# Performance work log

Measured on AMD Instinct MI355X. Metric: run time of the kernel, lower is better.

Reference implementation:

```python
import jax, jax.numpy as jnp
import numpy as np

B, R, U, D = 16, 2048, 2048, 1024
EPS_ATT = 1e-8
EPS_LN = 1e-6


def setup_inputs() -> dict:
    key = jax.random.key(0)
    ks = jax.random.split(key, 6)
    s = 1.0 / np.sqrt(D)
    return {
        "Q": jax.random.normal(ks[0], (B, R, D), dtype=jnp.float32),
        "K": jax.random.normal(ks[1], (B, U, D), dtype=jnp.float32),
        "V": jax.random.normal(ks[2], (B, U, D), dtype=jnp.float32),
        "W1": jax.random.normal(ks[3], (D, D), dtype=jnp.float32) * s,
        "b1": jnp.zeros((D,), dtype=jnp.float32),
        "W2": jax.random.normal(ks[4], (D, D), dtype=jnp.float32) * s,
        "b2": jnp.zeros((D,), dtype=jnp.float32),
        "gamma": jnp.ones((D,), dtype=jnp.float32),
        "beta": jnp.zeros((D,), dtype=jnp.float32),
    }


def reference(Q, K, V, W1, b1, W2, b2, gamma, beta):
    d_model = Q.shape[-1]
    # Faithful to source: sqrt(d_model + epsilon)
    scale = jnp.sqrt(jnp.asarray(d_model, jnp.float32) + EPS_ATT)
    scores = jnp.einsum('brd,bud->bru', Q, K) / scale  # [B,R,U]
    att = jax.nn.softmax(scores, axis=-1)
    V_att = jnp.einsum('bru,bud->brd', att, V)  # [B,R,D]

    def layer_norm(x):
        mu = jnp.mean(x, axis=-1, keepdims=True)
        var = jnp.mean(jnp.square(x - mu), axis=-1, keepdims=True)
        return gamma * (x - mu) / jnp.sqrt(var + EPS_LN) + beta

    X = layer_norm(Q + V_att)
    ffn = jnp.maximum(X @ W1 + b1, 0.0) @ W2 + b2
    return layer_norm(ffn + X)
```

## Files before the change

### kernel.cpp

```cpp
#include <hip/hip_runtime.h>
#include <math.h>
#include <stdint.h>

#define BATCH 16
#define RDIM 2048
#define UDIM 2048
#define DDIM 1024

typedef __attribute__((ext_vector_type(8))) short short8;
typedef __attribute__((ext_vector_type(4))) float f32x4;
typedef __attribute__((ext_vector_type(8))) unsigned short ushort8;
typedef __attribute__((ext_vector_type(4))) unsigned short ushort4v;
typedef __attribute__((ext_vector_type(4))) float float4v;

__device__ __forceinline__ float bf2f(unsigned short u) {
  unsigned int x = ((unsigned int)u) << 16;
  return __builtin_bit_cast(float, x);
}
__device__ __forceinline__ unsigned short f2bf(float f) {
  unsigned int x = __builtin_bit_cast(unsigned int, f);
  unsigned int r = (x + 0x7fffu + ((x >> 16) & 1u)) >> 16;
  return (unsigned short)r;
}

__device__ __forceinline__ void gload_lds16(const void* g, void* l) {
  __builtin_amdgcn_global_load_lds(
      (const __attribute__((address_space(1))) void*)(uintptr_t)g,
      (__attribute__((address_space(3))) void*)(uint32_t)(uintptr_t)l,
      16, 0, 0);
}


__global__ __launch_bounds__(256) void k_conv_bf16(const float* __restrict__ in,
                                                   unsigned short* __restrict__ out,
                                                   float scale) {
  const long i = ((long)blockIdx.x * 256 + threadIdx.x) * 8;
  float4v a = *(const float4v*)(in + i);
  float4v b = *(const float4v*)(in + i + 4);
  ushort8 o;
#pragma unroll
  for (int j = 0; j < 4; ++j) o[j] = f2bf(a[j] * scale);
#pragma unroll
  for (int j = 0; j < 4; ++j) o[4 + j] = f2bf(b[j] * scale);
  *(ushort8*)(out + i) = o;
}

__global__ void k_transpose_bf16(const float* __restrict__ in,
                                 unsigned short* __restrict__ out,
                                 int rows, int cols, long sIn, long sOut) {
  __shared__ unsigned short tile[64][65];
  const long bz = blockIdx.z;
  in += bz * sIn;
  out += bz * sOut;
  const int r0 = blockIdx.x * 64;
  const int c0 = blockIdx.y * 64;
  const int tx = threadIdx.x;
  const int ty = threadIdx.y;
#pragma unroll
  for (int i = 0; i < 16; ++i) {
    const int r = ty + i * 4;
    tile[r][tx] = f2bf(in[(long)(r0 + r) * cols + c0 + tx]);
  }
  __syncthreads();
#pragma unroll
  for (int i = 0; i < 16; ++i) {
    const int r = ty + i * 4;
    out[(long)(c0 + r) * rows + r0 + tx] = tile[tx][r];
  }
}


template <int EPI>
__global__ __launch_bounds__(512, 2) void gemm_bt(
    const unsigned short* __restrict__ A, const unsigned short* __restrict__ B,
    void* __restrict__ Cout, int N, int K, long sA, long sB, long sC,
    const float* __restrict__ bias, const unsigned short* __restrict__ res) {
  __shared__ __align__(32) unsigned short As[2][256 * 64];
  __shared__ __align__(32) unsigned short Bs[2][256 * 64];

  const int bz = blockIdx.z;
  const unsigned short* Ab = A + (long)bz * sA;
  const unsigned short* Bb = B + (long)bz * sB;

  const int tid = threadIdx.x;
  const int w = tid >> 6;
  const int lane = tid & 63;
  const int wm = w >> 2;
  const int wn = w & 3;
  const long rowBase = (long)blockIdx.x * 256;
  const long colBase = (long)blockIdx.y * 256;

  const int stR = w * 32 + (lane >> 3);
  const int stC = ((lane & 7) ^ (lane >> 3)) << 3;
  const unsigned short* gA0 = Ab + (rowBase + stR) * (long)K + stC;
  const unsigned short* gB0 = Bb + (colBase + stR) * (long)K + stC;
  char* lA0 = (char*)&As[0][0] + w * 4096;
  char* lB0 = (char*)&Bs[0][0] + w * 4096;

  auto STAGE = [&](int slot, int kt) {
    const unsigned short* ga = gA0 + (long)kt * 64;
    const unsigned short* gb = gB0 + (long)kt * 64;
    char* la = lA0 + slot * 32768;
    char* lb = lB0 + slot * 32768;
#pragma unroll
    for (int q = 0; q < 4; ++q) {
      gload_lds16(ga + (long)q * 8 * K, la + q * 1024);
      gload_lds16(gb + (long)q * 8 * K, lb + q * 1024);
    }
  };

  const int laneM = lane & 15;
  const int laneQ = lane >> 4;
  const int co0 = (laneQ << 4) ^ ((laneM & 7) << 4);

  f32x4 acc[8][4] = {};

  const int NT = K >> 6;
  STAGE(0, 0);
  STAGE(1, 1);
  asm volatile("s_waitcnt vmcnt(8)" ::: "memory");
  __builtin_amdgcn_s_barrier();

  for (int t = 0; t < NT; ++t) {
    const int cur = t & 1;
    const char* Ap = (const char*)&As[cur][0] + (wm * 128 + laneM) * 128;
    const char* Bp = (const char*)&Bs[cur][0] + (wn * 64 + laneM) * 128;

    short8 a[8][2], b[4][2];
#pragma unroll
    for (int ks = 0; ks < 2; ++ks) {
      const int co = co0 ^ (ks << 6);
#pragma unroll
      for (int m = 0; m < 4; ++m) a[m][ks] = *(const short8*)(Ap + m * 2048 + co);
#pragma unroll
      for (int n = 0; n < 4; ++n) b[n][ks] = *(const short8*)(Bp + n * 2048 + co);
#pragma unroll
      for (int m = 4; m < 8; ++m) a[m][ks] = *(const short8*)(Ap + m * 2048 + co);
    }
#pragma unroll
    for (int m = 0; m < 4; ++m)
#pragma unroll
      for (int n = 0; n < 4; ++n)
#pragma unroll
        for (int ks = 0; ks < 2; ++ks)
          acc[m][n] = __builtin_amdgcn_mfma_f32_16x16x32_bf16(a[m][ks], b[n][ks],
                                                              acc[m][n], 0, 0, 0);
    asm volatile("s_waitcnt lgkmcnt(0)" ::: "memory");
    __builtin_amdgcn_s_barrier();
    if (t + 2 < NT) STAGE(cur, t + 2);
    __builtin_amdgcn_s_setprio(1);
#pragma unroll
    for (int m = 4; m < 8; ++m)
#pragma unroll
      for (int n = 0; n < 4; ++n)
#pragma unroll
        for (int ks = 0; ks < 2; ++ks)
          acc[m][n] = __builtin_amdgcn_mfma_f32_16x16x32_bf16(a[m][ks], b[n][ks],
                                                              acc[m][n], 0, 0, 0);
    __builtin_amdgcn_s_setprio(0);
    if (t + 2 < NT) {
      asm volatile("s_waitcnt vmcnt(8)" ::: "memory");
    } else {
      asm volatile("s_waitcnt vmcnt(0)" ::: "memory");
    }
    __builtin_amdgcn_s_barrier();
  }

  const long r0 = rowBase + wm * 128;
  const long c0 = colBase + wn * 64;
  const int cr = (lane >> 4) << 2;
  const int cc = lane & 15;

  if constexpr (EPI == 0) {
    unsigned short* C = (unsigned short*)Cout + (long)bz * sC;
#pragma unroll
    for (int i = 0; i < 8; ++i)
#pragma unroll
      for (int j = 0; j < 4; ++j)
#pragma unroll
        for (int jj = 0; jj < 4; ++jj)
          C[(r0 + i * 16 + cr + jj) * N + (c0 + j * 16 + cc)] = f2bf(acc[i][j][jj]);
  } else if constexpr (EPI == 1) {
    unsigned short* C = (unsigned short*)Cout;
#pragma unroll
    for (int i = 0; i < 8; ++i)
#pragma unroll
      for (int j = 0; j < 4; ++j)
#pragma unroll
        for (int jj = 0; jj < 4; ++jj) {
          const long col = c0 + j * 16 + cc;
          float v = acc[i][j][jj] + bias[col];
          v = fmaxf(v, 0.f);
          C[(r0 + i * 16 + cr + jj) * N + col] = f2bf(v);
        }
  } else {
    float* C = (float*)Cout;
#pragma unroll
    for (int i = 0; i < 8; ++i)
#pragma unroll
      for (int j = 0; j < 4; ++j)
#pragma unroll
        for (int jj = 0; jj < 4; ++jj) {
          const long row = r0 + i * 16 + cr + jj;
          const long col = c0 + j * 16 + cc;
          C[row * N + col] = acc[i][j][jj] + bias[col] + bf2f(res[row * N + col]);
        }
  }
}


__global__ __launch_bounds__(256) void k_softmax(unsigned short* __restrict__ S) {
  __shared__ float red[8];
  const long base = (long)blockIdx.x * UDIM;
  const int t = threadIdx.x;
  ushort8 raw = *(const ushort8*)(S + base + t * 8);
  float v[8];
  float mx = -3.0e38f;
#pragma unroll
  for (int j = 0; j < 8; ++j) {
    v[j] = bf2f(raw[j]);
    mx = fmaxf(mx, v[j]);
  }
#pragma unroll
  for (int m = 32; m >= 1; m >>= 1) mx = fmaxf(mx, __shfl_xor(mx, m));
  const int wv = t >> 6;
  if ((t & 63) == 0) red[wv] = mx;
  __syncthreads();
  mx = fmaxf(fmaxf(red[0], red[1]), fmaxf(red[2], red[3]));
  float s = 0.f;
#pragma unroll
  for (int j = 0; j < 8; ++j) {
    v[j] = __expf(v[j] - mx);
    s += v[j];
  }
#pragma unroll
  for (int m = 32; m >= 1; m >>= 1) s += __shfl_xor(s, m);
  if ((t & 63) == 0) red[4 + wv] = s;
  __syncthreads();
  s = red[4] + red[5] + red[6] + red[7];
  const float rs = 1.f / s;
  ushort8 o;
#pragma unroll
  for (int j = 0; j < 8; ++j) o[j] = f2bf(v[j] * rs);
  *(ushort8*)(S + base + t * 8) = o;
}


__global__ __launch_bounds__(256) void k_addln_bf16(
    const float* __restrict__ Q, const unsigned short* __restrict__ Va,
    unsigned short* __restrict__ X, const float* __restrict__ gamma,
    const float* __restrict__ beta) {
  __shared__ float red[8];
  const long base = (long)blockIdx.x * DDIM;
  const int t = threadIdx.x;
  float4v q = *(const float4v*)(Q + base + t * 4);
  ushort4v a = *(const ushort4v*)(Va + base + t * 4);
  float x[4];
  float s = 0.f, ss = 0.f;
#pragma unroll
  for (int j = 0; j < 4; ++j) {
    x[j] = q[j] + bf2f(a[j]);
    s += x[j];
    ss += x[j] * x[j];
  }
#pragma unroll
  for (int m = 32; m >= 1; m >>= 1) {
    s += __shfl_xor(s, m);
    ss += __shfl_xor(ss, m);
  }
  const int wv = t >> 6;
  if ((t & 63) == 0) {
    red[wv] = s;
    red[4 + wv] = ss;
  }
  __syncthreads();
  s = red[0] + red[1] + red[2] + red[3];
  ss = red[4] + red[5] + red[6] + red[7];
  const float mu = s * (1.f / DDIM);
  const float var = ss * (1.f / DDIM) - mu * mu;
  const float rstd = rsqrtf(var + 1e-6f);
  ushort4v o;
#pragma unroll
  for (int j = 0; j < 4; ++j) {
    const int c = t * 4 + j;
    o[j] = f2bf(gamma[c] * ((x[j] - mu) * rstd) + beta[c]);
  }
  *(ushort4v*)(X + base + t * 4) = o;
}


__global__ __launch_bounds__(256) void k_ln_inplace(float* __restrict__ Y,
                                                    const float* __restrict__ gamma,
                                                    const float* __restrict__ beta) {
  __shared__ float red[8];
  const long base = (long)blockIdx.x * DDIM;
  const int t = threadIdx.x;
  float4v y = *(const float4v*)(Y + base + t * 4);
  float s = 0.f, ss = 0.f;
#pragma unroll
  for (int j = 0; j < 4; ++j) {
    s += y[j];
    ss += y[j] * y[j];
  }
#pragma unroll
  for (int m = 32; m >= 1; m >>= 1) {
    s += __shfl_xor(s, m);
    ss += __shfl_xor(ss, m);
  }
  const int wv = t >> 6;
  if ((t & 63) == 0) {
    red[wv] = s;
    red[4 + wv] = ss;
  }
  __syncthreads();
  s = red[0] + red[1] + red[2] + red[3];
  ss = red[4] + red[5] + red[6] + red[7];
  const float mu = s * (1.f / DDIM);
  const float var = ss * (1.f / DDIM) - mu * mu;
  const float rstd = rsqrtf(var + 1e-6f);
  float4v o;
#pragma unroll
  for (int j = 0; j < 4; ++j) {
    const int c = t * 4 + j;
    o[j] = gamma[c] * ((y[j] - mu) * rstd) + beta[c];
  }
  *(float4v*)(Y + base + t * 4) = o;
}


extern "C" void kernel_launch(void* const* d_in, const int* in_sizes, int n_in,
                              void* d_out, int out_size, void* d_ws, size_t ws_size,
                              hipStream_t stream) {
  const float* Q = (const float*)d_in[0];
  const float* Kin = (const float*)d_in[1];
  const float* V = (const float*)d_in[2];
  const float* W1 = (const float*)d_in[3];
  const float* b1 = (const float*)d_in[4];
  const float* W2 = (const float*)d_in[5];
  const float* b2 = (const float*)d_in[6];
  const float* gamma = (const float*)d_in[7];
  const float* beta = (const float*)d_in[8];
  float* out = (float*)d_out;

  const long nQ = (long)BATCH * RDIM * DDIM;
  const long nK = (long)BATCH * UDIM * DDIM;
  const long nS = (long)BATCH * RDIM * UDIM;

  char* w = (char*)d_ws;
  unsigned short* Qb = (unsigned short*)w;  w += nQ * 2;
  unsigned short* Kb = (unsigned short*)w;  w += nK * 2;
  unsigned short* Vt = (unsigned short*)w;  w += nK * 2;
  unsigned short* S  = (unsigned short*)w;  w += nS * 2;
  unsigned short* X  = (unsigned short*)w;  w += nQ * 2;
  unsigned short* W1t = (unsigned short*)w; w += (long)DDIM * DDIM * 2;
  unsigned short* W2t = (unsigned short*)w; w += (long)DDIM * DDIM * 2;
  unsigned short* Va = Qb;
  unsigned short* H  = S;

  const float scale = 1.0f / sqrtf(1024.0f + 1e-8f);

  k_conv_bf16<<<nQ / 2048, 256, 0, stream>>>(Q, Qb, scale);
  k_conv_bf16<<<nK / 2048, 256, 0, stream>>>(Kin, Kb, 1.0f);
  k_transpose_bf16<<<dim3(UDIM / 64, DDIM / 64, BATCH), dim3(64, 4), 0, stream>>>(
      V, Vt, UDIM, DDIM, (long)UDIM * DDIM, (long)UDIM * DDIM);
  k_transpose_bf16<<<dim3(DDIM / 64, DDIM / 64, 1), dim3(64, 4), 0, stream>>>(
      W1, W1t, DDIM, DDIM, 0, 0);
  k_transpose_bf16<<<dim3(DDIM / 64, DDIM / 64, 1), dim3(64, 4), 0, stream>>>(
      W2, W2t, DDIM, DDIM, 0, 0);

  gemm_bt<0><<<dim3(RDIM / 256, UDIM / 256, BATCH), 512, 0, stream>>>(
      Qb, Kb, S, UDIM, DDIM, (long)RDIM * DDIM, (long)UDIM * DDIM, (long)RDIM * UDIM,
      nullptr, nullptr);
  k_softmax<<<BATCH * RDIM, 256, 0, stream>>>(S);
  gemm_bt<0><<<dim3(RDIM / 256, DDIM / 256, BATCH), 512, 0, stream>>>(
      S, Vt, Va, DDIM, UDIM, (long)RDIM * UDIM, (long)DDIM * UDIM, (long)RDIM * DDIM,
      nullptr, nullptr);
  k_addln_bf16<<<BATCH * RDIM, 256, 0, stream>>>(Q, Va, X, gamma, beta);
  gemm_bt<1><<<dim3(BATCH * RDIM / 256, DDIM / 256, 1), 512, 0, stream>>>(
      X, W1t, H, DDIM, DDIM, 0, 0, 0, b1, nullptr);
  gemm_bt<2><<<dim3(BATCH * RDIM / 256, DDIM / 256, 1), 512, 0, stream>>>(
      H, W2t, out, DDIM, DDIM, 0, 0, 0, b2, X);
  k_ln_inplace<<<BATCH * RDIM, 256, 0, stream>>>(out, gamma, beta);
}
```

Baseline: 701.7 us.

## Restructure GEMM mainloop into four-phase k-half pipeline with interleaved staging

Splits each 64-wide K tile into two 32-wide halves stored in separate LDS slabs, and reorganizes the mainloop into four phases. Each phase loads a fragment subset from LDS, issues one global-to-LDS stage, and then runs an MFMA block. Scheduling fences and barriers are placed between phases so that global loads overlap compute at a finer grain and fewer fragment registers are live. This drops the XOR swizzle, which risks LDS bank conflicts, and adds more barriers per iteration. Loads past the last tile are clamped to the final tile instead of being skipped.

```diff
diff --git a/kernel.cpp b/kernel.cpp
--- a/kernel.cpp
+++ b/kernel.cpp
@@ -29,6 +29,11 @@
       (__attribute__((address_space(3))) void*)(uint32_t)(uintptr_t)l,
       16, 0, 0);
 }
+
+#define FENCE() __builtin_amdgcn_sched_barrier(0)
+#define BAR() __builtin_amdgcn_s_barrier()
+#define LGKM0() asm volatile("s_waitcnt lgkmcnt(0)" ::: "memory")
+#define VMCNT8() asm volatile("s_waitcnt vmcnt(8)" ::: "memory")
 
 
 __global__ __launch_bounds__(256) void k_conv_bf16(const float* __restrict__ in,
@@ -75,8 +80,7 @@
     const unsigned short* __restrict__ A, const unsigned short* __restrict__ B,
     void* __restrict__ Cout, int N, int K, long sA, long sB, long sC,
     const float* __restrict__ bias, const unsigned short* __restrict__ res) {
-  __shared__ __align__(32) unsigned short As[2][256 * 64];
-  __shared__ __align__(32) unsigned short Bs[2][256 * 64];
+  __shared__ __align__(128) unsigned short lds[2][2][2][256 * 32];
 
   const int bz = blockIdx.z;
   const unsigned short* Ab = A + (long)bz * sA;
@@ -90,80 +94,132 @@
   const long rowBase = (long)blockIdx.x * 256;
   const long colBase = (long)blockIdx.y * 256;
 
-  const int stR = w * 32 + (lane >> 3);
-  const int stC = ((lane & 7) ^ (lane >> 3)) << 3;
-  const unsigned short* gA0 = Ab + (rowBase + stR) * (long)K + stC;
-  const unsigned short* gB0 = Bb + (colBase + stR) * (long)K + stC;
-  char* lA0 = (char*)&As[0][0] + w * 4096;
-  char* lB0 = (char*)&Bs[0][0] + w * 4096;
-
-  auto STAGE = [&](int slot, int kt) {
-    const unsigned short* ga = gA0 + (long)kt * 64;
-    const unsigned short* gb = gB0 + (long)kt * 64;
-    char* la = lA0 + slot * 32768;
-    char* lb = lB0 + slot * 32768;
-#pragma unroll
-    for (int q = 0; q < 4; ++q) {
-      gload_lds16(ga + (long)q * 8 * K, la + q * 1024);
-      gload_lds16(gb + (long)q * 8 * K, lb + q * 1024);
-    }
+  const int stRow = w * 16 + (lane >> 2);
+  const int stKc = (lane & 3) << 3;
+  const unsigned short* gA = Ab + (rowBase + stRow) * (long)K + stKc;
+  const unsigned short* gB = Bb + (colBase + stRow) * (long)K + stKc;
+  const long qStep = (long)128 * K;
+  char* ldsB = (char*)&lds[0][0][0][0];
+  const int dOff = w * 1024;
+
+  auto STAGE = [&](int buf, int op, int ks, int kadd) {
+    const unsigned short* g = (op == 0 ? gA : gB) + kadd;
+    char* d = ldsB + ((buf * 4 + op * 2 + ks) << 14) + dOff;
+    gload_lds16(g, d);
+    gload_lds16(g + qStep, d + 8192);
   };
 
   const int laneM = lane & 15;
   const int laneQ = lane >> 4;
-  const int co0 = (laneQ << 4) ^ ((laneM & 7) << 4);
+  const int rdA = (wm * 128 + laneM) * 64 + laneQ * 16;
+  const int rdB = (wn * 64 + laneM) * 64 + laneQ * 16;
 
   f32x4 acc[8][4] = {};
-
   const int NT = K >> 6;
-  STAGE(0, 0);
-  STAGE(1, 1);
-  asm volatile("s_waitcnt vmcnt(8)" ::: "memory");
-  __builtin_amdgcn_s_barrier();
+  const int NTm1 = NT - 1;
+
+  STAGE(0, 0, 0, 0);
+  STAGE(0, 1, 0, 0);
+  STAGE(0, 0, 1, 32);
+  STAGE(0, 1, 1, 32);
+  STAGE(1, 0, 0, 64);
+  STAGE(1, 1, 0, 64);
+  VMCNT8();
+  BAR();
+  FENCE();
 
   for (int t = 0; t < NT; ++t) {
     const int cur = t & 1;
-    const char* Ap = (const char*)&As[cur][0] + (wm * 128 + laneM) * 128;
-    const char* Bp = (const char*)&Bs[cur][0] + (wn * 64 + laneM) * 128;
-
-    short8 a[8][2], b[4][2];
-#pragma unroll
-    for (int ks = 0; ks < 2; ++ks) {
-      const int co = co0 ^ (ks << 6);
-#pragma unroll
-      for (int m = 0; m < 4; ++m) a[m][ks] = *(const short8*)(Ap + m * 2048 + co);
-#pragma unroll
-      for (int n = 0; n < 4; ++n) b[n][ks] = *(const short8*)(Bp + n * 2048 + co);
-#pragma unroll
-      for (int m = 4; m < 8; ++m) a[m][ks] = *(const short8*)(Ap + m * 2048 + co);
-    }
+    const int sA0 = (cur * 4 + 0) << 14;
+    const int sA1 = (cur * 4 + 1) << 14;
+    const int sB0 = (cur * 4 + 2) << 14;
+    const int sB1 = (cur * 4 + 3) << 14;
+    const int t1 = (t + 1 <= NTm1 ? t + 1 : NTm1);
+    const int t2 = (t + 2 <= NTm1 ? t + 2 : NTm1);
+    const int k1add = t1 * 64 + 32;
+    const int k0add = t2 * 64;
+
+    short8 a0[4], a1[4], b0[4];
+
+#pragma unroll
+    for (int m = 0; m < 4; ++m)
+      a0[m] = *(const short8*)(ldsB + sA0 + rdA + m * 1024);
+#pragma unroll
+    for (int n = 0; n < 4; ++n)
+      b0[n] = *(const short8*)(ldsB + sB0 + rdB + n * 1024);
+    STAGE(cur ^ 1, 0, 1, k1add);
+    LGKM0();
+    FENCE();
+    __builtin_amdgcn_s_setprio(1);
 #pragma unroll
     for (int m = 0; m < 4; ++m)
 #pragma unroll
       for (int n = 0; n < 4; ++n)
-#pragma unroll
-        for (int ks = 0; ks < 2; ++ks)
-          acc[m][n] = __builtin_amdgcn_mfma_f32_16x16x32_bf16(a[m][ks], b[n][ks],
-                                                              acc[m][n], 0, 0, 0);
-    asm volatile("s_waitcnt lgkmcnt(0)" ::: "memory");
-    __builtin_amdgcn_s_barrier();
-    if (t + 2 < NT) STAGE(cur, t + 2);
+        acc[m][n] = __builtin_amdgcn_mfma_f32_16x16x32_bf16(a0[m], b0[n],
+                                                            acc[m][n], 0, 0, 0);
+    __builtin_amdgcn_s_setprio(0);
+    FENCE();
+    BAR();
+    FENCE();
+
+#pragma unroll
+    for (int m = 0; m < 4; ++m)
+      a1[m] = *(const short8*)(ldsB + sA0 + rdA + (4 + m) * 1024);
+    STAGE(cur ^ 1, 1, 1, k1add);
+    LGKM0();
+    FENCE();
     __builtin_amdgcn_s_setprio(1);
 #pragma unroll
-    for (int m = 4; m < 8; ++m)
+    for (int m = 0; m < 4; ++m)
 #pragma unroll
       for (int n = 0; n < 4; ++n)
-#pragma unroll
-        for (int ks = 0; ks < 2; ++ks)
-          acc[m][n] = __builtin_amdgcn_mfma_f32_16x16x32_bf16(a[m][ks], b[n][ks],
-                                                              acc[m][n], 0, 0, 0);
+        acc[4 + m][n] = __builtin_amdgcn_mfma_f32_16x16x32_bf16(a1[m], b0[n],
+                                                                acc[4 + m][n], 0, 0, 0);
     __builtin_amdgcn_s_setprio(0);
-    if (t + 2 < NT) {
-      asm volatile("s_waitcnt vmcnt(8)" ::: "memory");
-    } else {
-      asm volatile("s_waitcnt vmcnt(0)" ::: "memory");
-    }
-    __builtin_amdgcn_s_barrier();
+    FENCE();
+    VMCNT8();
+    BAR();
+    FENCE();
+
+#pragma unroll
+    for (int m = 0; m < 4; ++m)
+      a0[m] = *(const short8*)(ldsB + sA1 + rdA + m * 1024);
+#pragma unroll
+    for (int n = 0; n < 4; ++n)
+      b0[n] = *(const short8*)(ldsB + sB1 + rdB + n * 1024);
+    STAGE(cur, 0, 0, k0add);
+    LGKM0();
+    FENCE();
+    __builtin_amdgcn_s_setprio(1);
+#pragma unroll
+    for (int m = 0; m < 4; ++m)
+#pragma unroll
+      for (int n = 0; n < 4; ++n)
+        acc[m][n] = __builtin_amdgcn_mfma_f32_16x16x32_bf16(a0[m], b0[n],
+                                                            acc[m][n], 0, 0, 0);
+    __builtin_amdgcn_s_setprio(0);
+    FENCE();
+    BAR();
+    FENCE();
+
+#pragma unroll
+    for (int m = 0; m < 4; ++m)
+      a1[m] = *(const short8*)(ldsB + sA1 + rdA + (4 + m) * 1024);
+    STAGE(cur, 1, 0, k0add);
+    LGKM0();
+    FENCE();
+    __builtin_amdgcn_s_setprio(1);
+#pragma unroll
+    for (int m = 0; m < 4; ++m)
+#pragma unroll
+      for (int n = 0; n < 4; ++n)
+        acc[4 + m][n] = __builtin_amdgcn_mfma_f32_16x16x32_bf16(a1[m], b0[n],
+                                                                acc[4 + m][n], 0, 0, 0);
+    __builtin_amdgcn_s_setprio(0);
+    FENCE();
+    VMCNT8();
+    BAR();
+    FENCE();
   }
 
   const long r0 = rowBase + wm * 128;
```

Result: no change. 707.2 us (+0.8%).

## Restructure GEMM mainloop into 8-phase ping-pong schedule with split LDS halves

Applied to the files above, without the earlier changes.

Rewrites the bf16 GEMM main loop as an unrolled two-tile, eight-phase schedule. Each phase interleaves quarter-tile LDS reads, global-to-LDS prefetch of sub-halves and MFMA quadrants under explicit waitcnt and barrier control. LDS is re-laid out into k-split halves with a new XOR swizzle. Block indices are remapped with an 8-way interleave for cache locality, and launch bounds drop to one block per CU. The goal is better overlap of memory and MFMA, at the cost of many more barriers, lower occupancy, and reliance on exact vmcnt counts for correctness.

```diff
diff --git a/kernel.cpp b/kernel.cpp
--- a/kernel.cpp
+++ b/kernel.cpp
@@ -29,6 +29,13 @@
       (__attribute__((address_space(3))) void*)(uint32_t)(uintptr_t)l,
       16, 0, 0);
 }
+
+#define FENCE() __builtin_amdgcn_sched_barrier(0)
+#define BAR() __builtin_amdgcn_s_barrier()
+#define LGKM0() asm volatile("s_waitcnt lgkmcnt(0)" ::: "memory")
+#define LGKM8() asm volatile("s_waitcnt lgkmcnt(8)" ::: "memory")
+#define VMCNT6() asm volatile("s_waitcnt vmcnt(6)" ::: "memory")
+#define VMCNT0() asm volatile("s_waitcnt vmcnt(0)" ::: "memory")
 
 
 __global__ __launch_bounds__(256) void k_conv_bf16(const float* __restrict__ in,
@@ -71,14 +78,19 @@
 
 
 template <int EPI>
-__global__ __launch_bounds__(512, 2) void gemm_bt(
+__global__ __launch_bounds__(512, 1) void gemm_bt(
     const unsigned short* __restrict__ A, const unsigned short* __restrict__ B,
     void* __restrict__ Cout, int N, int K, long sA, long sB, long sC,
     const float* __restrict__ bias, const unsigned short* __restrict__ res) {
-  __shared__ __align__(32) unsigned short As[2][256 * 64];
-  __shared__ __align__(32) unsigned short Bs[2][256 * 64];
-
-  const int bz = blockIdx.z;
+  __shared__ __align__(128) unsigned short lds[2][2][2][256 * 32];
+
+  int lin = blockIdx.x + gridDim.x * (blockIdx.y + gridDim.y * blockIdx.z);
+  lin = (lin & 7) * ((gridDim.x * gridDim.y * gridDim.z) >> 3) + (lin >> 3);
+  const int by = lin % gridDim.y;
+  int rest = lin / gridDim.y;
+  const int bx = rest % gridDim.x;
+  const int bz = rest / gridDim.x;
+
   const unsigned short* Ab = A + (long)bz * sA;
   const unsigned short* Bb = B + (long)bz * sB;
 
@@ -87,84 +99,128 @@
   const int lane = tid & 63;
   const int wm = w >> 2;
   const int wn = w & 3;
-  const long rowBase = (long)blockIdx.x * 256;
-  const long colBase = (long)blockIdx.y * 256;
-
-  const int stR = w * 32 + (lane >> 3);
-  const int stC = ((lane & 7) ^ (lane >> 3)) << 3;
-  const unsigned short* gA0 = Ab + (rowBase + stR) * (long)K + stC;
-  const unsigned short* gB0 = Bb + (colBase + stR) * (long)K + stC;
-  char* lA0 = (char*)&As[0][0] + w * 4096;
-  char* lB0 = (char*)&Bs[0][0] + w * 4096;
-
-  auto STAGE = [&](int slot, int kt) {
-    const unsigned short* ga = gA0 + (long)kt * 64;
-    const unsigned short* gb = gB0 + (long)kt * 64;
-    char* la = lA0 + slot * 32768;
-    char* lb = lB0 + slot * 32768;
-#pragma unroll
-    for (int q = 0; q < 4; ++q) {
-      gload_lds16(ga + (long)q * 8 * K, la + q * 1024);
-      gload_lds16(gb + (long)q * 8 * K, lb + q * 1024);
-    }
+  const long rowBase = (long)bx * 256;
+  const long colBase = (long)by * 256;
+
+  const int s = tid >> 2;
+  const int kslot = (tid & 3) ^ ((tid >> 3) & 3);
+  const int lRowA = s + (s & 64);
+  const int lRowB = ((s & 96) << 1) + (s & 31);
+  const unsigned short* gA0 = Ab + (long)(rowBase + lRowA) * K + kslot * 8;
+  const unsigned short* gB0 = Bb + (long)(colBase + lRowB) * K + kslot * 8;
+  char* ldsB = (char*)&lds[0][0][0][0];
+  const int wOff = w * 1024;
+
+  auto STAGE_A = [&](int buf, int h, int kt) {
+    const unsigned short* g = gA0 + (long)(h * 64) * K + kt * 64;
+    char* d = ldsB + ((buf * 4 + 0) << 14) + h * 8192 + wOff;
+    gload_lds16(g, d);
+    gload_lds16(g + 32, d + 16384);
+  };
+  auto STAGE_B = [&](int buf, int h, int kt) {
+    const unsigned short* g = gB0 + (long)(h * 32) * K + kt * 64;
+    char* d = ldsB + ((buf * 4 + 2) << 14) + h * 8192 + wOff;
+    gload_lds16(g, d);
+    gload_lds16(g + 32, d + 16384);
   };
 
   const int laneM = lane & 15;
   const int laneQ = lane >> 4;
-  const int co0 = (laneQ << 4) ^ ((laneM & 7) << 4);
+  const int swz = (laneQ ^ ((laneM >> 1) & 3)) << 4;
+  const int rdA = (wm * 64 + laneM) * 64 + swz;
+  const int rdB = (wn * 32 + laneM) * 64 + swz;
 
   f32x4 acc[8][4] = {};
-
   const int NT = K >> 6;
-  STAGE(0, 0);
-  STAGE(1, 1);
-  asm volatile("s_waitcnt vmcnt(8)" ::: "memory");
-  __builtin_amdgcn_s_barrier();
-
-  for (int t = 0; t < NT; ++t) {
-    const int cur = t & 1;
-    const char* Ap = (const char*)&As[cur][0] + (wm * 128 + laneM) * 128;
-    const char* Bp = (const char*)&Bs[cur][0] + (wn * 64 + laneM) * 128;
-
-    short8 a[8][2], b[4][2];
-#pragma unroll
-    for (int ks = 0; ks < 2; ++ks) {
-      const int co = co0 ^ (ks << 6);
-#pragma unroll
-      for (int m = 0; m < 4; ++m) a[m][ks] = *(const short8*)(Ap + m * 2048 + co);
-#pragma unroll
-      for (int n = 0; n < 4; ++n) b[n][ks] = *(const short8*)(Bp + n * 2048 + co);
-#pragma unroll
-      for (int m = 4; m < 8; ++m) a[m][ks] = *(const short8*)(Ap + m * 2048 + co);
-    }
-#pragma unroll
-    for (int m = 0; m < 4; ++m)
-#pragma unroll
-      for (int n = 0; n < 4; ++n)
-#pragma unroll
-        for (int ks = 0; ks < 2; ++ks)
-          acc[m][n] = __builtin_amdgcn_mfma_f32_16x16x32_bf16(a[m][ks], b[n][ks],
-                                                              acc[m][n], 0, 0, 0);
-    asm volatile("s_waitcnt lgkmcnt(0)" ::: "memory");
-    __builtin_amdgcn_s_barrier();
-    if (t + 2 < NT) STAGE(cur, t + 2);
-    __builtin_amdgcn_s_setprio(1);
-#pragma unroll
-    for (int m = 4; m < 8; ++m)
-#pragma unroll
-      for (int n = 0; n < 4; ++n)
-#pragma unroll
-        for (int ks = 0; ks < 2; ++ks)
-          acc[m][n] = __builtin_amdgcn_mfma_f32_16x16x32_bf16(a[m][ks], b[n][ks],
-                                                              acc[m][n], 0, 0, 0);
-    __builtin_amdgcn_s_setprio(0);
-    if (t + 2 < NT) {
-      asm volatile("s_waitcnt vmcnt(8)" ::: "memory");
-    } else {
-      asm volatile("s_waitcnt vmcnt(0)" ::: "memory");
-    }
-    __builtin_amdgcn_s_barrier();
-  }
+  const int NI = NT >> 1;
+
+  short8 A0[4][2], A1[4][2], B0[2][2], B1[2][2];
+
+  auto RD_A = [&](short8 (&dst)[4][2], int buf, int h) {
+#pragma unroll
+    for (int mm = 0; mm < 4; ++mm)
+#pragma unroll
+      for (int kk = 0; kk < 2; ++kk)
+        dst[mm][kk] = *(const short8*)(ldsB + ((buf * 4 + kk) << 14) +
+                                       h * 8192 + rdA + mm * 1024);
+  };
+  auto RD_B = [&](short8 (&dst)[2][2], int buf, int h) {
+#pragma unroll
+    for (int nn = 0; nn < 2; ++nn)
+#pragma unroll
+      for (int kk = 0; kk < 2; ++kk)
+        dst[nn][kk] = *(const short8*)(ldsB + ((buf * 4 + 2 + kk) << 14) +
+                                       h * 8192 + rdB + nn * 1024);
+  };
+
+#define MFMAQ(AF, BF, MB, NB)                                                  \
+  __builtin_amdgcn_s_setprio(1);                                               \
+  _Pragma("unroll") for (int mm = 0; mm < 4; ++mm)                             \
+  _Pragma("unroll") for (int nn = 0; nn < 2; ++nn)                             \
+  _Pragma("unroll") for (int kk = 0; kk < 2; ++kk)                             \
+      acc[MB + mm][NB + nn] = __builtin_amdgcn_mfma_f32_16x16x32_bf16(         \
+          AF[mm][kk], BF[nn][kk], acc[MB + mm][NB + nn], 0, 0, 0);             \
+  __builtin_amdgcn_s_setprio(0);
+
+  STAGE_A(0, 0, 0); STAGE_B(0, 0, 0); STAGE_B(0, 1, 0); STAGE_A(0, 1, 0);
+  STAGE_A(1, 0, 1); STAGE_B(1, 0, 1); STAGE_B(1, 1, 1);
+  VMCNT6();
+  BAR();
+  FENCE();
+
+  for (int i = 0; i < NI; ++i) {
+    const int t1 = 2 * i + 1;
+    const int t2 = (2 * i + 2 <= NT - 1) ? 2 * i + 2 : NT - 1;
+    const int t3 = (2 * i + 3 <= NT - 1) ? 2 * i + 3 : NT - 1;
+
+    RD_A(A0, 0, 0); RD_B(B0, 0, 0);
+    STAGE_A(1, 1, t1);
+    LGKM8(); BAR(); LGKM0(); FENCE();
+    MFMAQ(A0, B0, 0, 0);
+    BAR();
+
+    RD_B(B1, 0, 1);
+    STAGE_A(0, 0, t2);
+    BAR(); LGKM0(); FENCE();
+    MFMAQ(A0, B1, 0, 2);
+    BAR();
+
+    RD_A(A1, 0, 1);
+    STAGE_B(0, 0, t2);
+    BAR(); LGKM0(); FENCE();
+    MFMAQ(A1, B1, 4, 2);
+    BAR();
+
+    STAGE_B(0, 1, t2);
+    VMCNT6(); BAR(); FENCE();
+    MFMAQ(A1, B0, 4, 0);
+    BAR();
+
+    RD_A(A0, 1, 0); RD_B(B0, 1, 0);
+    STAGE_A(0, 1, t2);
+    LGKM8(); BAR(); LGKM0(); FENCE();
+    MFMAQ(A0, B0, 0, 0);
+    BAR();
+
+    RD_B(B1, 1, 1);
+    STAGE_A(1, 0, t3);
+    BAR(); LGKM0(); FENCE();
+    MFMAQ(A0, B1, 0, 2);
+    BAR();
+
+    RD_A(A1, 1, 1);
+    STAGE_B(1, 0, t3);
+    BAR(); LGKM0(); FENCE();
+    MFMAQ(A1, B1, 4, 2);
+    BAR();
+
+    STAGE_B(1, 1, t3);
+    VMCNT6(); BAR(); FENCE();
+    MFMAQ(A1, B0, 4, 0);
+    BAR();
+  }
+  VMCNT0();
+#undef MFMAQ
 
   const long r0 = rowBase + wm * 128;
   const long c0 = colBase + wn * 64;
```

New measurement: 660.0 us. 5.9% less time.
